# Performance work log

Measured on AMD Instinct MI355X. Metric: run time of the kernel, lower is better.

Reference implementation:

```python
import jax, jax.numpy as jnp
import numpy as np

N, E, R, D, DEPTH = 50000, 800000, 1000, 128, 2


def setup_inputs() -> dict:
    key = jax.random.key(0)
    ks = jax.random.split(key, 6)
    features = jax.random.normal(ks[0], (N, D), jnp.float32)
    rel_emb = jax.random.normal(ks[1], (R, D), jnp.float32)
    # adj coalesced by row (torch coalesce sorts indices; values stay aligned)
    src = jnp.sort(jax.random.randint(ks[2], (E,), 0, N))
    dst = jax.random.randint(ks[3], (E,), 0, N)
    adj = jnp.stack([src, dst]).astype(jnp.int64)
    # one relation per triple: row index = triple id, col = relation id
    r_index = jnp.stack([jnp.arange(E), jax.random.randint(ks[4], (E,), 0, R)]).astype(jnp.int64)
    r_val = jax.random.uniform(ks[5], (E,), jnp.float32)
    attn_kernels = jax.random.normal(jax.random.fold_in(key, 7), (DEPTH, D), jnp.float32) * 0.1
    return {"features": features, "rel_emb": rel_emb, "adj": adj, "r_index": r_index,
            "r_val": r_val, "triple_size": E, "rel_size": R, "node_size": N,
            "attn_kernels": attn_kernels}


def _layer(features, rel_emb, adj, r_index, r_val, triple_size, node_size, attn_k):
    row = adj[0]
    neighs = features[adj[1]]                                   # [E, D] gather
    # sparse.mm(tri_rel, rel_emb): sum_j r_val * rel_emb[col] per triple row
    tri_rel = jax.ops.segment_sum(r_val[:, None] * rel_emb[r_index[1]],
                                  r_index[0], num_segments=triple_size)  # [E, D]
    nrm = jnp.linalg.norm(tri_rel, axis=1, keepdims=True)
    tri_rel = tri_rel / jnp.maximum(nrm, 1e-12)                 # F.normalize(p=2)
    # Householder-style reflection
    neighs = neighs - 2.0 * jnp.sum(neighs * tri_rel, axis=1, keepdims=True) * tri_rel
    att = tri_rel @ attn_k                                      # [E]
    # sparse row-wise softmax over edges grouped by destination row
    m = jax.ops.segment_max(att, row, num_segments=node_size)
    e = jnp.exp(att - m[row])
    s = jax.ops.segment_sum(e, row, num_segments=node_size)
    att = e / s[row]
    new_features = jax.ops.segment_sum(neighs * att[:, None], row,
                                       num_segments=node_size)  # [N, D] scatter
    return jnp.tanh(new_features)


def reference(features, rel_emb, adj, r_index, r_val, triple_size, rel_size, node_size, attn_kernels):
    features = jnp.tanh(features)
    outputs = [features]
    for l in range(attn_kernels.shape[0]):
        features = _layer(features, rel_emb, adj, r_index, r_val,
                          triple_size, node_size, attn_kernels[l])
        outputs.append(features)
    return jnp.concatenate(outputs, axis=-1)                    # [N, D*(depth+1)]
```

## Files before the change

### kernel.cpp

```cpp
#include <hip/hip_runtime.h>
#include <hip/hip_bf16.h>
#include <math.h>

#define N_NODES   50000
#define N_EDGES   800000
#define N_REL     1000
#define DIM       128
#define DEPTH_L   2
#define OUT_STRIDE (DIM * (DEPTH_L + 1))

typedef _Float16 h2 __attribute__((ext_vector_type(2)));

#if defined(__has_builtin)
#if __has_builtin(__builtin_amdgcn_fdot2)
#define FDOT2(a, b, c) __builtin_amdgcn_fdot2((a), (b), (c), false)
#endif
#endif
#ifndef FDOT2
#define FDOT2(a, b, c) ((c) + (float)(a).x * (float)(b).x + (float)(a).y * (float)(b).y)
#endif

__device__ __forceinline__ float fast_tanh(float x) {
    float cx = fminf(fmaxf(x, -15.f), 15.f);
    float e = __expf(2.f * cx);
    return (e - 1.f) * __frcp_rn(e + 1.f);
}

__global__ __launch_bounds__(64) void prep_rel_kernel(
    const float* __restrict__ rel_emb,
    const float* __restrict__ attn_k,
    _Float16* __restrict__ rhat,
    float* __restrict__ att_rel)
{
    int r = blockIdx.x;
    int lane = threadIdx.x;
    if (r == N_REL) {
        rhat[(size_t)r * DIM + lane]      = (_Float16)0.f;
        rhat[(size_t)r * DIM + lane + 64] = (_Float16)0.f;
        if (lane < DEPTH_L) att_rel[lane * (N_REL + 1) + N_REL] = 0.f;
        return;
    }
    float v0 = rel_emb[r * DIM + lane];
    float v1 = rel_emb[r * DIM + lane + 64];
    float ss = v0 * v0 + v1 * v1;
    #pragma unroll
    for (int o = 32; o >= 1; o >>= 1) ss += __shfl_xor(ss, o);
    float inv = 1.0f / fmaxf(sqrtf(ss), 1e-12f);
    float t0 = v0 * inv, t1 = v1 * inv;
    rhat[(size_t)r * DIM + lane]      = (_Float16)t0;
    rhat[(size_t)r * DIM + lane + 64] = (_Float16)t1;
    #pragma unroll
    for (int l = 0; l < DEPTH_L; ++l) {
        float d = t0 * attn_k[l * DIM + lane] + t1 * attn_k[l * DIM + lane + 64];
        #pragma unroll
        for (int o = 32; o >= 1; o >>= 1) d += __shfl_xor(d, o);
        if (lane == 0) att_rel[l * (N_REL + 1) + r] = d;
    }
}

__global__ __launch_bounds__(256) void rowptr_kernel(
    const int* __restrict__ src, int* __restrict__ rp)
{
    int n = blockIdx.x * blockDim.x + threadIdx.x;
    if (n > N_NODES) return;
    int lo = 0, hi = N_EDGES;
    while (lo < hi) {
        int mid = (lo + hi) >> 1;
        if (src[mid] < n) lo = mid + 1; else hi = mid;
    }
    rp[n] = lo;
}

__global__ __launch_bounds__(256) void tanh0_kernel(
    const float* __restrict__ feat, float* __restrict__ out,
    _Float16* __restrict__ fs0)
{
    int i = blockIdx.x * blockDim.x + threadIdx.x;
    if (i >= N_NODES * 32) return;
    int n = i >> 5;
    int j = i & 31;
    float4 v = reinterpret_cast<const float4*>(feat + (size_t)n * DIM)[j];
    float4 o;
    o.x = fast_tanh(v.x); o.y = fast_tanh(v.y);
    o.z = fast_tanh(v.z); o.w = fast_tanh(v.w);
    reinterpret_cast<float4*>(out + (size_t)n * OUT_STRIDE)[j] = o;
    h2 p0; p0.x = (_Float16)o.x; p0.y = (_Float16)o.y;
    h2 p1; p1.x = (_Float16)o.z; p1.y = (_Float16)o.w;
    uint2 u;
    u.x = __builtin_bit_cast(unsigned, p0);
    u.y = __builtin_bit_cast(unsigned, p1);
    reinterpret_cast<uint2*>(fs0 + (size_t)n * DIM)[j] = u;
}

__global__ __launch_bounds__(128) void stats_kernel(
    const int* __restrict__ relid, const float* __restrict__ rval,
    const int* __restrict__ rp, const float* __restrict__ att_rel,
    float4* __restrict__ ms)
{
    int wid  = threadIdx.x >> 6;
    int lane = threadIdx.x & 63;
    int node = blockIdx.x * 2 + wid;
    if (node >= N_NODES) return;
    int start = rp[node], end = rp[node + 1];
    if (start >= end) return;
    const float* ar0 = att_rel;
    const float* ar1 = att_rel + (N_REL + 1);

    float m0 = -INFINITY, s0 = 0.f, m1 = -INFINITY, s1 = 0.f;
    for (int e = start + lane; e < end; e += 64) {
        int r = (rval[e] == 0.f) ? N_REL : relid[e];
        float l0 = ar0[r], l1 = ar1[r];
        if (l0 > m0) { s0 = s0 * __expf(m0 - l0) + 1.f; m0 = l0; }
        else         { s0 += __expf(l0 - m0); }
        if (l1 > m1) { s1 = s1 * __expf(m1 - l1) + 1.f; m1 = l1; }
        else         { s1 += __expf(l1 - m1); }
    }
    #pragma unroll
    for (int o = 32; o >= 1; o >>= 1) {
        float ma = __shfl_xor(m0, o), sa = __shfl_xor(s0, o);
        float mn = fmaxf(m0, ma);
        s0 = (mn == -INFINITY) ? 0.f : s0 * __expf(m0 - mn) + sa * __expf(ma - mn);
        m0 = mn;
        float mb = __shfl_xor(m1, o), sb = __shfl_xor(s1, o);
        float mo = fmaxf(m1, mb);
        s1 = (mo == -INFINITY) ? 0.f : s1 * __expf(m1 - mo) + sb * __expf(mb - mo);
        m1 = mo;
    }
    if (lane == 0)
        ms[node] = make_float4(m0, 1.0f / s0, m1, 1.0f / s1);
}

__global__ __launch_bounds__(256) void einfo_kernel(
    const int* __restrict__ src, const int* __restrict__ dst,
    const int* __restrict__ relid, const float* __restrict__ rval,
    const float* __restrict__ att_rel, const float4* __restrict__ ms,
    uint2* __restrict__ einfo2)
{
    int e = blockIdx.x * 256 + threadIdx.x;
    if (e >= N_EDGES) return;
    int r = (rval[e] == 0.f) ? N_REL : relid[e];
    float4 m = ms[src[e]];
    float w0 = __expf(att_rel[r] - m.x) * m.y;
    float w1 = __expf(att_rel[(N_REL + 1) + r] - m.z) * m.w;
    h2 wp; wp.x = (_Float16)w0; wp.y = (_Float16)w1;
    einfo2[e] = make_uint2((unsigned)dst[e] | ((unsigned)r << 16),
                           __builtin_bit_cast(unsigned, wp));
}

template<int L>
__global__ __launch_bounds__(128) void layer_fused_kernel(
    const _Float16* __restrict__ fs_in,
    float* __restrict__ fout,
    _Float16* __restrict__ fs_out,
    const uint2* __restrict__ einfo2,
    const int* __restrict__ rp,
    const _Float16* __restrict__ rhat)
{
    int wid  = threadIdx.x >> 6;
    int lane = threadIdx.x & 63;
    int node = blockIdx.x * 2 + wid;
    if (node >= N_NODES) return;
    int start = rp[node], end = rp[node + 1];
    int g = lane >> 3;
    int q = lane & 7;

    const char* fbase = (const char*)fs_in + 32 * q;
    const char* tbase = (const char*)rhat  + 32 * q;
    int g0 = (lane >> 3) & 1, g1 = (lane >> 4) & 1, g2 = (lane >> 5) & 1;

    h2 a2[8];
    #pragma unroll
    for (int i = 0; i < 8; ++i) { a2[i].x = (_Float16)0.f; a2[i].y = (_Float16)0.f; }

    for (int e0 = start; e0 < end; e0 += 8) {
        int e = e0 + g;
        bool valid = (e < end);
        int ec = valid ? e : (end - 1);
        uint2 ei = einfo2[ec];
        unsigned dn = ei.x & 0xffffu;
        unsigned rl = ei.x >> 16;
        h2 wp = __builtin_bit_cast(h2, ei.y);
        _Float16 w = valid ? ((L == 0) ? wp.x : wp.y) : (_Float16)0.f;

        const uint4* hp = reinterpret_cast<const uint4*>(fbase + (size_t)dn * 256);
        const uint4* tp = reinterpret_cast<const uint4*>(tbase + (size_t)rl * 256);
        uint4 hu0 = hp[0], hu1 = hp[1];
        uint4 tu0 = tp[0], tu1 = tp[1];

        h2 hh[8], tt[8];
        hh[0] = __builtin_bit_cast(h2, hu0.x); hh[1] = __builtin_bit_cast(h2, hu0.y);
        hh[2] = __builtin_bit_cast(h2, hu0.z); hh[3] = __builtin_bit_cast(h2, hu0.w);
        hh[4] = __builtin_bit_cast(h2, hu1.x); hh[5] = __builtin_bit_cast(h2, hu1.y);
        hh[6] = __builtin_bit_cast(h2, hu1.z); hh[7] = __builtin_bit_cast(h2, hu1.w);
        tt[0] = __builtin_bit_cast(h2, tu0.x); tt[1] = __builtin_bit_cast(h2, tu0.y);
        tt[2] = __builtin_bit_cast(h2, tu0.z); tt[3] = __builtin_bit_cast(h2, tu0.w);
        tt[4] = __builtin_bit_cast(h2, tu1.x); tt[5] = __builtin_bit_cast(h2, tu1.y);
        tt[6] = __builtin_bit_cast(h2, tu1.z); tt[7] = __builtin_bit_cast(h2, tu1.w);

        float d0 = 0.f, d1 = 0.f;
        #pragma unroll
        for (int p = 0; p < 8; p += 2) {
            d0 = FDOT2(hh[p],     tt[p],     d0);
            d1 = FDOT2(hh[p + 1], tt[p + 1], d1);
        }
        float d = d0 + d1;
        d += __shfl_xor(d, 1);
        d += __shfl_xor(d, 2);
        d += __shfl_xor(d, 4);
        float cf = -2.f * (float)w * d;
        _Float16 cfh = (_Float16)cf;
        h2 wv; wv.x = w;   wv.y = w;
        h2 cv; cv.x = cfh; cv.y = cfh;

        #pragma unroll
        for (int p = 0; p < 8; ++p) {
            a2[p] = hh[p] * wv + a2[p];
            a2[p] = tt[p] * cv + a2[p];
        }
    }

    h2 b1[4];
    #pragma unroll
    for (int k = 0; k < 4; ++k) {
        h2 keep = g0 ? a2[2*k + 1] : a2[2*k];
        h2 send = g0 ? a2[2*k] : a2[2*k + 1];
        unsigned su = __shfl_xor(__builtin_bit_cast(unsigned, send), 8);
        b1[k] = keep + __builtin_bit_cast(h2, su);
    }
    h2 b2[2];
    #pragma unroll
    for (int m = 0; m < 2; ++m) {
        h2 keep = g1 ? b1[2*m + 1] : b1[2*m];
        h2 send = g1 ? b1[2*m] : b1[2*m + 1];
        unsigned su = __shfl_xor(__builtin_bit_cast(unsigned, send), 16);
        b2[m] = keep + __builtin_bit_cast(h2, su);
    }
    h2 c;
    {
        h2 keep = g2 ? b2[1] : b2[0];
        h2 send = g2 ? b2[0] : b2[1];
        unsigned su = __shfl_xor(__builtin_bit_cast(unsigned, send), 32);
        c = keep + __builtin_bit_cast(h2, su);
    }

    float y0 = fast_tanh((float)c.x), y1 = fast_tanh((float)c.y);
    int dimo = 16 * q + 2 * g;
    *reinterpret_cast<float2*>(fout + (size_t)node * OUT_STRIDE + dimo)
        = make_float2(y0, y1);
    if (L == 0) {
        h2 pr; pr.x = (_Float16)y0; pr.y = (_Float16)y1;
        *reinterpret_cast<h2*>(fs_out + (size_t)node * DIM + dimo) = pr;
    }
}

extern "C" void kernel_launch(void* const* d_in, const int* in_sizes, int n_in,
                              void* d_out, int out_size, void* d_ws, size_t ws_size,
                              hipStream_t stream)
{
    const float* features = (const float*)d_in[0];
    const float* rel_emb  = (const float*)d_in[1];
    const int*   adj      = (const int*)d_in[2];
    const int*   r_index  = (const int*)d_in[3];
    const float* r_val    = (const float*)d_in[4];
    const float* attn_k   = (const float*)d_in[8];
    float* out = (float*)d_out;

    const int* src   = adj;
    const int* dst   = adj + N_EDGES;
    const int* relid = r_index + N_EDGES;

    char* base = (char*)d_ws;
    _Float16* rhat    = (_Float16*)base;
    float*    att_rel = (float*)(base + 256256);
    int*      rp      = (int*)(base + 264264);
    float4*   ms      = (float4*)(base + 464272);
    uint2*    einfo2  = (uint2*)(base + 1264272);
    _Float16* fs0     = (_Float16*)(base + 1264272 + (size_t)N_EDGES * 8);
    _Float16* fs1     = fs0 + (size_t)N_NODES * DIM;

    prep_rel_kernel<<<N_REL + 1, 64, 0, stream>>>(rel_emb, attn_k, rhat, att_rel);
    rowptr_kernel<<<(N_NODES + 1 + 255) / 256, 256, 0, stream>>>(src, rp);
    tanh0_kernel<<<(N_NODES * 32 + 255) / 256, 256, 0, stream>>>(features, out, fs0);
    stats_kernel<<<(N_NODES + 1) / 2, 128, 0, stream>>>(relid, r_val, rp, att_rel, ms);
    einfo_kernel<<<(N_EDGES + 255) / 256, 256, 0, stream>>>(
        src, dst, relid, r_val, att_rel, ms, einfo2);

    layer_fused_kernel<0><<<(N_NODES + 1) / 2, 128, 0, stream>>>(
        fs0, out + 1 * DIM, fs1, einfo2, rp, rhat);
    layer_fused_kernel<1><<<(N_NODES + 1) / 2, 128, 0, stream>>>(
        fs1, out + 2 * DIM, fs0, einfo2, rp, rhat);
}
```

Measured before the change: 133.8 us.

## Fuse tanh, softmax stats and edge weights; interleave two nodes per wave

Merges the tanh0, stats and einfo kernels into a single per-node kernel. It computes the softmax max and sum, then writes the per-edge weights directly, which removes two launches and the intermediate ms buffer. The layer kernel now has each wavefront process two nodes with interleaved chunk loads, so more independent gathers are in flight per wave. In exchange, register pressure rises, and nodes with very different degrees leave a wave partly idle.

```diff
diff --git a/kernel.cpp b/kernel.cpp
--- a/kernel.cpp
+++ b/kernel.cpp
@@ -71,36 +71,26 @@
     rp[n] = lo;
 }
 
-__global__ __launch_bounds__(256) void tanh0_kernel(
+__global__ __launch_bounds__(128) void weights_tanh_kernel(
     const float* __restrict__ feat, float* __restrict__ out,
-    _Float16* __restrict__ fs0)
-{
-    int i = blockIdx.x * blockDim.x + threadIdx.x;
-    if (i >= N_NODES * 32) return;
-    int n = i >> 5;
-    int j = i & 31;
-    float4 v = reinterpret_cast<const float4*>(feat + (size_t)n * DIM)[j];
-    float4 o;
-    o.x = fast_tanh(v.x); o.y = fast_tanh(v.y);
-    o.z = fast_tanh(v.z); o.w = fast_tanh(v.w);
-    reinterpret_cast<float4*>(out + (size_t)n * OUT_STRIDE)[j] = o;
-    h2 p0; p0.x = (_Float16)o.x; p0.y = (_Float16)o.y;
-    h2 p1; p1.x = (_Float16)o.z; p1.y = (_Float16)o.w;
-    uint2 u;
-    u.x = __builtin_bit_cast(unsigned, p0);
-    u.y = __builtin_bit_cast(unsigned, p1);
-    reinterpret_cast<uint2*>(fs0 + (size_t)n * DIM)[j] = u;
-}
-
-__global__ __launch_bounds__(128) void stats_kernel(
-    const int* __restrict__ relid, const float* __restrict__ rval,
-    const int* __restrict__ rp, const float* __restrict__ att_rel,
-    float4* __restrict__ ms)
+    _Float16* __restrict__ fs0,
+    const int* __restrict__ dst, const int* __restrict__ relid,
+    const float* __restrict__ rval, const int* __restrict__ rp,
+    const float* __restrict__ att_rel,
+    uint2* __restrict__ einfo2)
 {
     int wid  = threadIdx.x >> 6;
     int lane = threadIdx.x & 63;
     int node = blockIdx.x * 2 + wid;
     if (node >= N_NODES) return;
+
+    float2 v = *reinterpret_cast<const float2*>(feat + (size_t)node * DIM + 2 * lane);
+    float y0 = fast_tanh(v.x), y1 = fast_tanh(v.y);
+    *reinterpret_cast<float2*>(out + (size_t)node * OUT_STRIDE + 2 * lane)
+        = make_float2(y0, y1);
+    h2 pr; pr.x = (_Float16)y0; pr.y = (_Float16)y1;
+    *reinterpret_cast<h2*>(fs0 + (size_t)node * DIM + 2 * lane) = pr;
+
     int start = rp[node], end = rp[node + 1];
     if (start >= end) return;
     const float* ar0 = att_rel;
@@ -126,99 +116,77 @@
         s1 = (mo == -INFINITY) ? 0.f : s1 * __expf(m1 - mo) + sb * __expf(mb - mo);
         m1 = mo;
     }
-    if (lane == 0)
-        ms[node] = make_float4(m0, 1.0f / s0, m1, 1.0f / s1);
-}
-
-__global__ __launch_bounds__(256) void einfo_kernel(
-    const int* __restrict__ src, const int* __restrict__ dst,
-    const int* __restrict__ relid, const float* __restrict__ rval,
-    const float* __restrict__ att_rel, const float4* __restrict__ ms,
-    uint2* __restrict__ einfo2)
-{
-    int e = blockIdx.x * 256 + threadIdx.x;
-    if (e >= N_EDGES) return;
-    int r = (rval[e] == 0.f) ? N_REL : relid[e];
-    float4 m = ms[src[e]];
-    float w0 = __expf(att_rel[r] - m.x) * m.y;
-    float w1 = __expf(att_rel[(N_REL + 1) + r] - m.z) * m.w;
-    h2 wp; wp.x = (_Float16)w0; wp.y = (_Float16)w1;
-    einfo2[e] = make_uint2((unsigned)dst[e] | ((unsigned)r << 16),
-                           __builtin_bit_cast(unsigned, wp));
-}
+    float i0 = 1.0f / s0, i1 = 1.0f / s1;
+    for (int e = start + lane; e < end; e += 64) {
+        int r = (rval[e] == 0.f) ? N_REL : relid[e];
+        float w0 = __expf(ar0[r] - m0) * i0;
+        float w1 = __expf(ar1[r] - m1) * i1;
+        h2 wp; wp.x = (_Float16)w0; wp.y = (_Float16)w1;
+        einfo2[e] = make_uint2((unsigned)dst[e] | ((unsigned)r << 16),
+                               __builtin_bit_cast(unsigned, wp));
+    }
+}
+
 
 template<int L>
-__global__ __launch_bounds__(128) void layer_fused_kernel(
-    const _Float16* __restrict__ fs_in,
-    float* __restrict__ fout,
-    _Float16* __restrict__ fs_out,
-    const uint2* __restrict__ einfo2,
-    const int* __restrict__ rp,
-    const _Float16* __restrict__ rhat)
-{
-    int wid  = threadIdx.x >> 6;
-    int lane = threadIdx.x & 63;
-    int node = blockIdx.x * 2 + wid;
-    if (node >= N_NODES) return;
-    int start = rp[node], end = rp[node + 1];
-    int g = lane >> 3;
-    int q = lane & 7;
-
-    const char* fbase = (const char*)fs_in + 32 * q;
-    const char* tbase = (const char*)rhat  + 32 * q;
-    int g0 = (lane >> 3) & 1, g1 = (lane >> 4) & 1, g2 = (lane >> 5) & 1;
-
-    h2 a2[8];
-    #pragma unroll
-    for (int i = 0; i < 8; ++i) { a2[i].x = (_Float16)0.f; a2[i].y = (_Float16)0.f; }
-
-    for (int e0 = start; e0 < end; e0 += 8) {
-        int e = e0 + g;
-        bool valid = (e < end);
-        int ec = valid ? e : (end - 1);
-        uint2 ei = einfo2[ec];
-        unsigned dn = ei.x & 0xffffu;
-        unsigned rl = ei.x >> 16;
-        h2 wp = __builtin_bit_cast(h2, ei.y);
-        _Float16 w = valid ? ((L == 0) ? wp.x : wp.y) : (_Float16)0.f;
-
-        const uint4* hp = reinterpret_cast<const uint4*>(fbase + (size_t)dn * 256);
-        const uint4* tp = reinterpret_cast<const uint4*>(tbase + (size_t)rl * 256);
-        uint4 hu0 = hp[0], hu1 = hp[1];
-        uint4 tu0 = tp[0], tu1 = tp[1];
-
-        h2 hh[8], tt[8];
-        hh[0] = __builtin_bit_cast(h2, hu0.x); hh[1] = __builtin_bit_cast(h2, hu0.y);
-        hh[2] = __builtin_bit_cast(h2, hu0.z); hh[3] = __builtin_bit_cast(h2, hu0.w);
-        hh[4] = __builtin_bit_cast(h2, hu1.x); hh[5] = __builtin_bit_cast(h2, hu1.y);
-        hh[6] = __builtin_bit_cast(h2, hu1.z); hh[7] = __builtin_bit_cast(h2, hu1.w);
-        tt[0] = __builtin_bit_cast(h2, tu0.x); tt[1] = __builtin_bit_cast(h2, tu0.y);
-        tt[2] = __builtin_bit_cast(h2, tu0.z); tt[3] = __builtin_bit_cast(h2, tu0.w);
-        tt[4] = __builtin_bit_cast(h2, tu1.x); tt[5] = __builtin_bit_cast(h2, tu1.y);
-        tt[6] = __builtin_bit_cast(h2, tu1.z); tt[7] = __builtin_bit_cast(h2, tu1.w);
-
-        float d0 = 0.f, d1 = 0.f;
-        #pragma unroll
-        for (int p = 0; p < 8; p += 2) {
-            d0 = FDOT2(hh[p],     tt[p],     d0);
-            d1 = FDOT2(hh[p + 1], tt[p + 1], d1);
-        }
-        float d = d0 + d1;
-        d += __shfl_xor(d, 1);
-        d += __shfl_xor(d, 2);
-        d += __shfl_xor(d, 4);
-        float cf = -2.f * (float)w * d;
-        _Float16 cfh = (_Float16)cf;
-        h2 wv; wv.x = w;   wv.y = w;
-        h2 cv; cv.x = cfh; cv.y = cfh;
-
-        #pragma unroll
-        for (int p = 0; p < 8; ++p) {
-            a2[p] = hh[p] * wv + a2[p];
-            a2[p] = tt[p] * cv + a2[p];
-        }
-    }
-
+__device__ __forceinline__ void chunk_load(
+    const uint2* __restrict__ einfo2, int e0, int g, int end,
+    const char* fbase, const char* tbase,
+    uint4& hu0, uint4& hu1, uint4& tu0, uint4& tu1, _Float16& w)
+{
+    int e = e0 + g;
+    bool valid = (e < end);
+    int ec = valid ? e : (end - 1);
+    uint2 ei = einfo2[ec];
+    unsigned dn = ei.x & 0xffffu;
+    unsigned rl = ei.x >> 16;
+    h2 wp = __builtin_bit_cast(h2, ei.y);
+    w = valid ? ((L == 0) ? wp.x : wp.y) : (_Float16)0.f;
+    const uint4* hp = reinterpret_cast<const uint4*>(fbase + (size_t)dn * 256);
+    const uint4* tp = reinterpret_cast<const uint4*>(tbase + (size_t)rl * 256);
+    hu0 = hp[0]; hu1 = hp[1];
+    tu0 = tp[0]; tu1 = tp[1];
+}
+
+__device__ __forceinline__ void chunk_compute(
+    uint4 hu0, uint4 hu1, uint4 tu0, uint4 tu1, _Float16 w, h2* a2)
+{
+    h2 hh[8], tt[8];
+    hh[0] = __builtin_bit_cast(h2, hu0.x); hh[1] = __builtin_bit_cast(h2, hu0.y);
+    hh[2] = __builtin_bit_cast(h2, hu0.z); hh[3] = __builtin_bit_cast(h2, hu0.w);
+    hh[4] = __builtin_bit_cast(h2, hu1.x); hh[5] = __builtin_bit_cast(h2, hu1.y);
+    hh[6] = __builtin_bit_cast(h2, hu1.z); hh[7] = __builtin_bit_cast(h2, hu1.w);
+    tt[0] = __builtin_bit_cast(h2, tu0.x); tt[1] = __builtin_bit_cast(h2, tu0.y);
+    tt[2] = __builtin_bit_cast(h2, tu0.z); tt[3] = __builtin_bit_cast(h2, tu0.w);
+    tt[4] = __builtin_bit_cast(h2, tu1.x); tt[5] = __builtin_bit_cast(h2, tu1.y);
+    tt[6] = __builtin_bit_cast(h2, tu1.z); tt[7] = __builtin_bit_cast(h2, tu1.w);
+
+    float d0 = 0.f, d1 = 0.f;
+    #pragma unroll
+    for (int p = 0; p < 8; p += 2) {
+        d0 = FDOT2(hh[p],     tt[p],     d0);
+        d1 = FDOT2(hh[p + 1], tt[p + 1], d1);
+    }
+    float d = d0 + d1;
+    d += __shfl_xor(d, 1);
+    d += __shfl_xor(d, 2);
+    d += __shfl_xor(d, 4);
+    float cf = -2.f * (float)w * d;
+    _Float16 cfh = (_Float16)cf;
+    h2 wv; wv.x = w;   wv.y = w;
+    h2 cv; cv.x = cfh; cv.y = cfh;
+    #pragma unroll
+    for (int p = 0; p < 8; ++p) {
+        a2[p] = hh[p] * wv + a2[p];
+        a2[p] = tt[p] * cv + a2[p];
+    }
+}
+
+template<int L>
+__device__ __forceinline__ void fold_write(
+    h2* a2, int g0, int g1, int g2, int q, int g, int node,
+    float* __restrict__ fout, _Float16* __restrict__ fs_out)
+{
     h2 b1[4];
     #pragma unroll
     for (int k = 0; k < 4; ++k) {
@@ -242,7 +210,6 @@
         unsigned su = __shfl_xor(__builtin_bit_cast(unsigned, send), 32);
         c = keep + __builtin_bit_cast(h2, su);
     }
-
     float y0 = fast_tanh((float)c.x), y1 = fast_tanh((float)c.y);
     int dimo = 16 * q + 2 * g;
     *reinterpret_cast<float2*>(fout + (size_t)node * OUT_STRIDE + dimo)
@@ -253,6 +220,54 @@
     }
 }
 
+template<int L>
+__global__ __launch_bounds__(128, 4) void layer_fused_kernel(
+    const _Float16* __restrict__ fs_in,
+    float* __restrict__ fout,
+    _Float16* __restrict__ fs_out,
+    const uint2* __restrict__ einfo2,
+    const int* __restrict__ rp,
+    const _Float16* __restrict__ rhat)
+{
+    int wid  = threadIdx.x >> 6;
+    int lane = threadIdx.x & 63;
+    int nA = blockIdx.x * 4 + wid * 2;
+    int nB = nA + 1;
+    if (nA >= N_NODES) return;
+    bool hasB = (nB < N_NODES);
+
+    int sA = rp[nA], eA = rp[nA + 1];
+    int sB = 0, eB = 0;
+    if (hasB) { sB = rp[nB]; eB = rp[nB + 1]; }
+
+    int g = lane >> 3;
+    int q = lane & 7;
+    const char* fbase = (const char*)fs_in + 32 * q;
+    const char* tbase = (const char*)rhat  + 32 * q;
+    int g0 = (lane >> 3) & 1, g1 = (lane >> 4) & 1, g2 = (lane >> 5) & 1;
+
+    h2 aA[8], aB[8];
+    #pragma unroll
+    for (int i = 0; i < 8; ++i) {
+        aA[i].x = (_Float16)0.f; aA[i].y = (_Float16)0.f;
+        aB[i].x = (_Float16)0.f; aB[i].y = (_Float16)0.f;
+    }
+
+    int cA = sA, cB = sB;
+    while (cA < eA || cB < eB) {
+        bool doA = (cA < eA), doB = (cB < eB);
+        uint4 hA0, hA1, tA0, tA1; _Float16 wA = (_Float16)0.f;
+        uint4 hB0, hB1, tB0, tB1; _Float16 wB = (_Float16)0.f;
+        if (doA) chunk_load<L>(einfo2, cA, g, eA, fbase, tbase, hA0, hA1, tA0, tA1, wA);
+        if (doB) chunk_load<L>(einfo2, cB, g, eB, fbase, tbase, hB0, hB1, tB0, tB1, wB);
+        if (doA) { chunk_compute(hA0, hA1, tA0, tA1, wA, aA); cA += 8; }
+        if (doB) { chunk_compute(hB0, hB1, tB0, tB1, wB, aB); cB += 8; }
+    }
+
+    fold_write<L>(aA, g0, g1, g2, q, g, nA, fout, fs_out);
+    if (hasB) fold_write<L>(aB, g0, g1, g2, q, g, nB, fout, fs_out);
+}
+
 extern "C" void kernel_launch(void* const* d_in, const int* in_sizes, int n_in,
                               void* d_out, int out_size, void* d_ws, size_t ws_size,
                               hipStream_t stream)
@@ -273,20 +288,17 @@
     _Float16* rhat    = (_Float16*)base;
     float*    att_rel = (float*)(base + 256256);
     int*      rp      = (int*)(base + 264264);
-    float4*   ms      = (float4*)(base + 464272);
-    uint2*    einfo2  = (uint2*)(base + 1264272);
-    _Float16* fs0     = (_Float16*)(base + 1264272 + (size_t)N_EDGES * 8);
+    uint2*    einfo2  = (uint2*)(base + 464272);
+    _Float16* fs0     = (_Float16*)(base + 464272 + (size_t)N_EDGES * 8);
     _Float16* fs1     = fs0 + (size_t)N_NODES * DIM;
 
     prep_rel_kernel<<<N_REL + 1, 64, 0, stream>>>(rel_emb, attn_k, rhat, att_rel);
     rowptr_kernel<<<(N_NODES + 1 + 255) / 256, 256, 0, stream>>>(src, rp);
-    tanh0_kernel<<<(N_NODES * 32 + 255) / 256, 256, 0, stream>>>(features, out, fs0);
-    stats_kernel<<<(N_NODES + 1) / 2, 128, 0, stream>>>(relid, r_val, rp, att_rel, ms);
-    einfo_kernel<<<(N_EDGES + 255) / 256, 256, 0, stream>>>(
-        src, dst, relid, r_val, att_rel, ms, einfo2);
-
-    layer_fused_kernel<0><<<(N_NODES + 1) / 2, 128, 0, stream>>>(
+    weights_tanh_kernel<<<(N_NODES + 1) / 2, 128, 0, stream>>>(
+        features, out, fs0, dst, relid, r_val, rp, att_rel, einfo2);
+
+    layer_fused_kernel<0><<<(N_NODES + 3) / 4, 128, 0, stream>>>(
         fs0, out + 1 * DIM, fs1, einfo2, rp, rhat);
-    layer_fused_kernel<1><<<(N_NODES + 1) / 2, 128, 0, stream>>>(
+    layer_fused_kernel<1><<<(N_NODES + 3) / 4, 128, 0, stream>>>(
         fs1, out + 2 * DIM, fs0, einfo2, rp, rhat);
 }
```

New measurement: 130.5 us. -2.5%, faster.
